# Optimization experiments

Hardware: AMD Instinct MI355X
Metric: run time of the kernel (lower is better)

## Reference

```python
import jax, jax.numpy as jnp
import numpy as np

C = 256          # input_dim
OUT = 256        # output_dim
DM = C // 4      # mamba d_model
DS = 16          # d_state
DC = 4           # d_conv
DI = 2 * DM      # d_inner (expand=2)
DTR = max(1, -(-DM // 16))  # dt_rank = ceil(d_model/16) = 4
B, Dd, H, W = 2, 8, 16, 32


def setup_inputs() -> dict:
    key = jax.random.key(0)
    ks = jax.random.split(key, 12)
    s = 0.02
    inp = {
        'x': jax.random.normal(ks[0], (B, C, Dd, H, W), jnp.float32),
        'ln_g': jnp.ones((C,), jnp.float32),
        'ln_b': jnp.zeros((C,), jnp.float32),
        'in_proj_w': jax.random.normal(ks[1], (2 * DI, DM), jnp.float32) * s,
        'conv_w': jax.random.normal(ks[2], (DI, DC), jnp.float32) * s,
        'conv_b': jnp.zeros((DI,), jnp.float32),
        'x_proj_w': jax.random.normal(ks[3], (DTR + 2 * DS, DI), jnp.float32) * s,
        'dt_proj_w': jax.random.normal(ks[4], (DI, DTR), jnp.float32) * s,
        'dt_proj_b': jax.random.uniform(ks[5], (DI,), jnp.float32, -4.0, -2.0),
        'A_log': jnp.log(jnp.broadcast_to(jnp.arange(1, DS + 1, dtype=jnp.float32), (DI, DS))),
        'D_param': jnp.ones((DI,), jnp.float32),
        'out_proj_w': jax.random.normal(ks[6], (DM, DI), jnp.float32) * s,
        'proj_w': jax.random.normal(ks[7], (OUT, C), jnp.float32) * s,
        'proj_b': jnp.zeros((OUT,), jnp.float32),
        'skip_scale': jnp.ones((1,), jnp.float32),
    }
    return inp


def _layernorm(h, g, b, eps=1e-5):
    mu = jnp.mean(h, axis=-1, keepdims=True)
    var = jnp.mean(jnp.square(h - mu), axis=-1, keepdims=True)
    return (h - mu) * jax.lax.rsqrt(var + eps) * g + b


def _mamba(xp, in_proj_w, conv_w, conv_b, x_proj_w, dt_proj_w, dt_proj_b, A_log, D_param, out_proj_w):
    # xp: (B, L, DM)
    xz = xp @ in_proj_w.T                      # (B, L, 2*DI)
    xc, z = jnp.split(xz, 2, axis=-1)
    # causal depthwise conv1d, kernel DC, left-pad DC-1
    xcT = xc.transpose(0, 2, 1)                # (B, DI, L)
    k = conv_w[:, None, :]                     # (DI, 1, DC)
    conv = jax.lax.conv_general_dilated(xcT, k, (1,), [(DC - 1, 0)], feature_group_count=DI)
    xc = jax.nn.silu(conv + conv_b[None, :, None]).transpose(0, 2, 1)  # (B, L, DI)
    x_dbl = xc @ x_proj_w.T                    # (B, L, DTR+2*DS)
    dt = x_dbl[..., :DTR]
    Bm = x_dbl[..., DTR:DTR + DS]
    Cm = x_dbl[..., DTR + DS:]
    dt = jax.nn.softplus(dt @ dt_proj_w.T + dt_proj_b)  # (B, L, DI)
    A = -jnp.exp(A_log)                        # (DI, DS)
    dA = jnp.exp(dt[..., None] * A)            # (B, L, DI, DS)
    dBx = dt[..., None] * Bm[:, :, None, :] * xc[..., None]  # (B, L, DI, DS)

    def step(h, inp):
        dA_t, dBx_t, C_t = inp
        h = dA_t * h + dBx_t                   # (B, DI, DS)
        y = jnp.einsum('bds,bs->bd', h, C_t)
        return h, y

    h0 = jnp.zeros((xp.shape[0], DI, DS), xp.dtype)
    _, ys = jax.lax.scan(step, h0, (dA.transpose(1, 0, 2, 3), dBx.transpose(1, 0, 2, 3), Cm.transpose(1, 0, 2)))
    y = ys.transpose(1, 0, 2) + D_param * xc   # (B, L, DI)
    y = y * jax.nn.silu(z)
    return y @ out_proj_w.T                    # (B, L, DM)


def reference(x, ln_g, ln_b, in_proj_w, conv_w, conv_b, x_proj_w, dt_proj_w, dt_proj_b,
              A_log, D_param, out_proj_w, proj_w, proj_b, skip_scale):
    Bb, Cc, Dd_, H_, W_ = x.shape
    L = Dd_ * H_ * W_
    xf = x.reshape(Bb, Cc, L).transpose(0, 2, 1)        # (B, L, C)
    xn = _layernorm(xf, ln_g, ln_b)
    parts = xn.reshape(Bb, L, 4, DM).transpose(2, 0, 1, 3)  # (4, B, L, DM), contiguous chunks
    mam = lambda p: _mamba(p, in_proj_w, conv_w, conv_b, x_proj_w, dt_proj_w,
                           dt_proj_b, A_log, D_param, out_proj_w)
    outs = jax.vmap(mam)(parts) + skip_scale * parts    # shared Mamba weights across chunks
    xm = outs.transpose(1, 2, 0, 3).reshape(Bb, L, Cc)
    xm = _layernorm(xm, ln_g, ln_b)                      # same LN module reused
    xp = (xm @ proj_w.T + proj_b).transpose(0, 2, 1)     # (B, OUT, L)
    return xp.reshape(Bb, -1, Dd_, H_, W_)
```

## Files before the change

### kernel.cpp

```cpp
#include <hip/hip_runtime.h>


#define B_    2
#define C_    256
#define L_    4096
#define P_    4
#define DM_   64
#define DI_   128
#define OUT_  256
#define NCH   128
#define CHL   32

__global__ __launch_bounds__(256) void k1_ln(const float* __restrict__ x,
        const float* __restrict__ g, const float* __restrict__ bb,
        float* __restrict__ xn) {
  __shared__ float tile[256][33];
  __shared__ float psum[8][32];
  __shared__ float psq[8][32];
  __shared__ float smu[32], srs[32];
  int t = threadIdx.x;
  int l0 = blockIdx.x * 32;
  int b = blockIdx.y;
  const float* xb = x + (size_t)b * C_ * L_;
  int ll = t & 31, cr = t >> 5;
  for (int i = 0; i < 32; ++i) {
    int c = cr + 8 * i;
    tile[c][ll] = xb[(size_t)c * L_ + l0 + ll];
  }
  __syncthreads();
  {
    int l = t & 31, k = t >> 5;
    float s = 0.f, sq = 0.f;
    #pragma unroll 8
    for (int j = 0; j < 32; ++j) {
      float v = tile[32 * k + j][l];
      s += v; sq += v * v;
    }
    psum[k][l] = s; psq[k][l] = sq;
  }
  __syncthreads();
  if (t < 32) {
    float s = 0.f, sq = 0.f;
    #pragma unroll
    for (int k = 0; k < 8; ++k) { s += psum[k][t]; sq += psq[k][t]; }
    float mu = s * (1.f / 256.f);
    float var = sq * (1.f / 256.f) - mu * mu;
    smu[t] = mu;
    srs[t] = rsqrtf(var + 1e-5f);
  }
  __syncthreads();
  float gc = g[t], bc = bb[t];
  for (int l = 0; l < 32; ++l) {
    float v = (tile[t][l] - smu[l]) * srs[l] * gc + bc;
    xn[((size_t)b * L_ + l0 + l) * C_ + t] = v;
  }
}

__global__ __launch_bounds__(256) void k2_inproj(const float* __restrict__ xn,
        const float* __restrict__ w, float* __restrict__ xz) {
  __shared__ float swT[32 * 256];
  __shared__ float sxT[32 * 64];
  int t = threadIdx.x;
  int l0 = blockIdx.x * 64;
  int p = blockIdx.y, b = blockIdx.z;
  int to = t & 63, tl = t >> 6;
  float acc[4][16];
  #pragma unroll
  for (int io = 0; io < 4; ++io)
    #pragma unroll
    for (int il = 0; il < 16; ++il) acc[io][il] = 0.f;

  for (int kt = 0; kt < 2; ++kt) {
    __syncthreads();
    {
      const float* wr = w + (size_t)t * 64 + kt * 32;
      #pragma unroll
      for (int k4 = 0; k4 < 8; ++k4) {
        float4 v = *(const float4*)&wr[k4 * 4];
        swT[(k4 * 4 + 0) * 256 + t] = v.x;
        swT[(k4 * 4 + 1) * 256 + t] = v.y;
        swT[(k4 * 4 + 2) * 256 + t] = v.z;
        swT[(k4 * 4 + 3) * 256 + t] = v.w;
      }
    }
    {
      int l = t & 63, dg = t >> 6;
      const float* xr = xn + ((size_t)b * L_ + l0 + l) * 256 + p * 64 + kt * 32 + dg * 8;
      #pragma unroll
      for (int jj = 0; jj < 2; ++jj) {
        float4 v = *(const float4*)&xr[jj * 4];
        sxT[(dg * 8 + jj * 4 + 0) * 64 + l] = v.x;
        sxT[(dg * 8 + jj * 4 + 1) * 64 + l] = v.y;
        sxT[(dg * 8 + jj * 4 + 2) * 64 + l] = v.z;
        sxT[(dg * 8 + jj * 4 + 3) * 64 + l] = v.w;
      }
    }
    __syncthreads();
    for (int k = 0; k < 32; ++k) {
      float4 b4 = *(const float4*)&swT[k * 256 + to * 4];
      #pragma unroll
      for (int q = 0; q < 4; ++q) {
        float4 a4 = *(const float4*)&sxT[k * 64 + tl * 16 + q * 4];
        acc[0][q*4+0] += b4.x * a4.x; acc[0][q*4+1] += b4.x * a4.y;
        acc[0][q*4+2] += b4.x * a4.z; acc[0][q*4+3] += b4.x * a4.w;
        acc[1][q*4+0] += b4.y * a4.x; acc[1][q*4+1] += b4.y * a4.y;
        acc[1][q*4+2] += b4.y * a4.z; acc[1][q*4+3] += b4.y * a4.w;
        acc[2][q*4+0] += b4.z * a4.x; acc[2][q*4+1] += b4.z * a4.y;
        acc[2][q*4+2] += b4.z * a4.z; acc[2][q*4+3] += b4.z * a4.w;
        acc[3][q*4+0] += b4.w * a4.x; acc[3][q*4+1] += b4.w * a4.y;
        acc[3][q*4+2] += b4.w * a4.z; acc[3][q*4+3] += b4.w * a4.w;
      }
    }
  }
  size_t ob = ((size_t)((b * 4 + p)) * L_ + l0 + tl * 16) * 256 + to * 4;
  #pragma unroll
  for (int il = 0; il < 16; ++il) {
    float4 v = make_float4(acc[0][il], acc[1][il], acc[2][il], acc[3][il]);
    *(float4*)&xz[ob + (size_t)il * 256] = v;
  }
}

__global__ __launch_bounds__(256) void k3_convdt(const float* __restrict__ xz,
        const float* __restrict__ conv_w, const float* __restrict__ conv_b,
        const float* __restrict__ x_proj_w, const float* __restrict__ dt_proj_w,
        const float* __restrict__ dt_proj_b,
        float* __restrict__ xc, float* __restrict__ dt, float* __restrict__ bc) {
  __shared__ float sxc[64 * 128];
  __shared__ float sdb[64 * 5];
  __shared__ float sbc[64 * 33];
  int t = threadIdx.x;
  int l0 = blockIdx.x * 64;
  int bp = blockIdx.z * P_ + blockIdx.y;
  const float* xzb = xz + (size_t)bp * L_ * 256;

  {
    int d = t & 127, lh = t >> 7;
    int lstart = l0 + lh * 32;
    float4 cw = *(const float4*)&conv_w[d * 4];
    float cb = conv_b[d];
    float w0 = (lstart >= 3) ? xzb[(size_t)(lstart - 3) * 256 + d] : 0.f;
    float w1 = (lstart >= 2) ? xzb[(size_t)(lstart - 2) * 256 + d] : 0.f;
    float w2 = (lstart >= 1) ? xzb[(size_t)(lstart - 1) * 256 + d] : 0.f;
    float* xcrow = xc + ((size_t)bp * L_ + lstart) * 128 + d;
    const float* xzrow = xzb + (size_t)lstart * 256 + d;
    #pragma unroll 4
    for (int i = 0; i < 32; ++i) {
      float w3 = xzrow[(size_t)i * 256];
      float cv = cb + cw.x * w0 + cw.y * w1 + cw.z * w2 + cw.w * w3;
      float sv = cv / (1.f + __expf(-cv));
      int row = lh * 32 + i;
      sxc[row * 128 + (d ^ (4 * (row & 31)))] = sv;
      xcrow[(size_t)i * 128] = sv;
      w0 = w1; w1 = w2; w2 = w3;
    }
  }
  __syncthreads();
  {
    int l = t & 63, og = t >> 6;
    float acc[9];
    #pragma unroll
    for (int rr = 0; rr < 9; ++rr) acc[rr] = 0.f;
    const float* wbase = x_proj_w + og * 9 * 128;
    for (int k4 = 0; k4 < 32; ++k4) {
      float4 a4 = *(const float4*)&sxc[l * 128 + ((k4 * 4) ^ (4 * (l & 31)))];
      #pragma unroll
      for (int rr = 0; rr < 9; ++rr) {
        float4 w4 = *(const float4*)&wbase[rr * 128 + k4 * 4];
        acc[rr] += a4.x * w4.x + a4.y * w4.y + a4.z * w4.z + a4.w * w4.w;
      }
    }
    #pragma unroll
    for (int rr = 0; rr < 9; ++rr) {
      int ra = og * 9 + rr;
      if (ra < 4) sdb[l * 5 + ra] = acc[rr];
      else sbc[l * 33 + (ra - 4)] = acc[rr];
    }
  }
  __syncthreads();
  #pragma unroll
  for (int i = 0; i < 8; ++i) {
    int idx = t + 256 * i;
    int row = idx >> 5, col = idx & 31;
    bc[((size_t)bp * L_ + l0 + row) * 32 + col] = sbc[row * 33 + col];
  }
  {
    int d = t & 127, lh = t >> 7;
    float4 dw = *(const float4*)&dt_proj_w[d * 4];
    float dpb = dt_proj_b[d];
    float* dtrow = dt + ((size_t)bp * L_ + l0 + lh * 32) * 128 + d;
    #pragma unroll 4
    for (int i = 0; i < 32; ++i) {
      int row = lh * 32 + i;
      float v = dpb + sdb[row * 5 + 0] * dw.x + sdb[row * 5 + 1] * dw.y
                    + sdb[row * 5 + 2] * dw.z + sdb[row * 5 + 3] * dw.w;
      float sp = (v > 20.f) ? v : log1pf(__expf(v));
      dtrow[(size_t)i * 128] = sp;
    }
  }
}

__global__ __launch_bounds__(128) void k4a_scanA(const float* __restrict__ dt,
        const float* __restrict__ xc, const float* __restrict__ bcbuf,
        const float* __restrict__ A_log,
        float* __restrict__ chA, float* __restrict__ chH) {
  int d = threadIdx.x;
  int ch = blockIdx.x, bp = blockIdx.y;
  float Av[16], h[16];
  #pragma unroll
  for (int q = 0; q < 4; ++q) {
    float4 a = *(const float4*)&A_log[d * 16 + q * 4];
    Av[q*4+0] = -__expf(a.x); Av[q*4+1] = -__expf(a.y);
    Av[q*4+2] = -__expf(a.z); Av[q*4+3] = -__expf(a.w);
  }
  #pragma unroll
  for (int s = 0; s < 16; ++s) h[s] = 0.f;
  float sumdt = 0.f;
  const float* dtp = dt + (size_t)bp * L_ * 128 + (size_t)ch * CHL * 128 + d;
  const float* xcp = xc + (size_t)bp * L_ * 128 + (size_t)ch * CHL * 128 + d;
  const float* bcp = bcbuf + (size_t)bp * L_ * 32 + (size_t)ch * CHL * 32;
  #pragma unroll 2
  for (int tt = 0; tt < CHL; ++tt) {
    float dtv = dtp[tt * 128];
    float xcv = xcp[tt * 128];
    float Bv[16];
    *(float4*)&Bv[0]  = *(const float4*)&bcp[tt * 32 + 0];
    *(float4*)&Bv[4]  = *(const float4*)&bcp[tt * 32 + 4];
    *(float4*)&Bv[8]  = *(const float4*)&bcp[tt * 32 + 8];
    *(float4*)&Bv[12] = *(const float4*)&bcp[tt * 32 + 12];
    float w = dtv * xcv;
    sumdt += dtv;
    #pragma unroll
    for (int s = 0; s < 16; ++s) {
      float dA = __expf(dtv * Av[s]);
      h[s] = fmaf(dA, h[s], w * Bv[s]);
    }
  }
  size_t o = (((size_t)bp * NCH + ch) * 128 + d) * 16;
  #pragma unroll
  for (int s = 0; s < 16; ++s) chA[o + s] = __expf(sumdt * Av[s]);
  #pragma unroll
  for (int s = 0; s < 16; ++s) chH[o + s] = h[s];
}

__global__ __launch_bounds__(256) void k4b_fold(const float* __restrict__ chA,
        float* __restrict__ chH) {
  int tid = blockIdx.x * 256 + threadIdx.x;
  int bp = tid >> 11;
  int rem = tid & 2047;
  float h = 0.f;
  for (int ch = 0; ch < NCH; ++ch) {
    size_t o = ((size_t)bp * NCH + ch) * 2048 + rem;
    float a = chA[o];
    float e = chH[o];
    chH[o] = h;
    h = fmaf(a, h, e);
  }
}

__global__ __launch_bounds__(128) void k5_scanB(const float* __restrict__ dt,
        const float* __restrict__ xc, const float* __restrict__ bcbuf,
        const float* __restrict__ xz, const float* __restrict__ A_log,
        const float* __restrict__ D_param, const float* __restrict__ chH,
        float* __restrict__ yg) {
  int d = threadIdx.x;
  int ch = blockIdx.x, bp = blockIdx.y;
  float Av[16], h[16];
  #pragma unroll
  for (int q = 0; q < 4; ++q) {
    float4 a = *(const float4*)&A_log[d * 16 + q * 4];
    Av[q*4+0] = -__expf(a.x); Av[q*4+1] = -__expf(a.y);
    Av[q*4+2] = -__expf(a.z); Av[q*4+3] = -__expf(a.w);
  }
  {
    size_t o = (((size_t)bp * NCH + ch) * 128 + d) * 16;
    #pragma unroll
    for (int q = 0; q < 4; ++q)
      *(float4*)&h[q * 4] = *(const float4*)&chH[o + q * 4];
  }
  float Dv = D_param[d];
  const float* dtp = dt + (size_t)bp * L_ * 128 + (size_t)ch * CHL * 128 + d;
  const float* xcp = xc + (size_t)bp * L_ * 128 + (size_t)ch * CHL * 128 + d;
  const float* bcp = bcbuf + (size_t)bp * L_ * 32 + (size_t)ch * CHL * 32;
  const float* zp  = xz + (size_t)bp * L_ * 256 + (size_t)ch * CHL * 256 + 128 + d;
  float* ygp = yg + (size_t)bp * L_ * 128 + (size_t)ch * CHL * 128 + d;
  #pragma unroll 2
  for (int tt = 0; tt < CHL; ++tt) {
    float dtv = dtp[tt * 128];
    float xcv = xcp[tt * 128];
    float zv  = zp[tt * 256];
    float Bv[16], Cv[16];
    *(float4*)&Bv[0]  = *(const float4*)&bcp[tt * 32 + 0];
    *(float4*)&Bv[4]  = *(const float4*)&bcp[tt * 32 + 4];
    *(float4*)&Bv[8]  = *(const float4*)&bcp[tt * 32 + 8];
    *(float4*)&Bv[12] = *(const float4*)&bcp[tt * 32 + 12];
    *(float4*)&Cv[0]  = *(const float4*)&bcp[tt * 32 + 16];
    *(float4*)&Cv[4]  = *(const float4*)&bcp[tt * 32 + 20];
    *(float4*)&Cv[8]  = *(const float4*)&bcp[tt * 32 + 24];
    *(float4*)&Cv[12] = *(const float4*)&bcp[tt * 32 + 28];
    float w = dtv * xcv;
    float r = 0.f;
    #pragma unroll
    for (int s = 0; s < 16; ++s) {
      float dA = __expf(dtv * Av[s]);
      h[s] = fmaf(dA, h[s], w * Bv[s]);
      r = fmaf(h[s], Cv[s], r);
    }
    float y = fmaf(Dv, xcv, r);
    float sig = 1.f / (1.f + __expf(-zv));
    ygp[tt * 128] = y * (zv * sig);
  }
}

__global__ __launch_bounds__(256) void k6a_gemm(const float* __restrict__ yg,
        const float* __restrict__ xn, const float* __restrict__ opw,
        const float* __restrict__ skip, float* __restrict__ xmn) {
  __shared__ float sgT[128 * 64];
  __shared__ float swT2[128 * 64];
  int t = threadIdx.x;
  int l0 = blockIdx.x * 64;
  int p = blockIdx.y, b = blockIdx.z;
  int bp = b * 4 + p;
  float sk = skip[0];
  {
    int l = t & 63, dg = t >> 6;
    const float* yr = yg + ((size_t)bp * L_ + l0 + l) * 128 + dg * 32;
    const float* wr = opw + (size_t)l * 128 + dg * 32;
    #pragma unroll
    for (int jj = 0; jj < 8; ++jj) {
      float4 v = *(const float4*)&yr[jj * 4];
      int dd = dg * 32 + jj * 4;
      sgT[(dd + 0) * 64 + l] = v.x; sgT[(dd + 1) * 64 + l] = v.y;
      sgT[(dd + 2) * 64 + l] = v.z; sgT[(dd + 3) * 64 + l] = v.w;
      float4 u = *(const float4*)&wr[jj * 4];
      swT2[(dd + 0) * 64 + l] = u.x; swT2[(dd + 1) * 64 + l] = u.y;
      swT2[(dd + 2) * 64 + l] = u.z; swT2[(dd + 3) * 64 + l] = u.w;
    }
  }
  __syncthreads();
  int to = t & 15, tl = t >> 4;
  float acc[4][4];
  #pragma unroll
  for (int io = 0; io < 4; ++io)
    #pragma unroll
    for (int il = 0; il < 4; ++il) acc[io][il] = 0.f;
  for (int dd = 0; dd < 128; ++dd) {
    float4 a4 = *(const float4*)&sgT[dd * 64 + tl * 4];
    float4 b4 = *(const float4*)&swT2[dd * 64 + to * 4];
    acc[0][0] += b4.x * a4.x; acc[0][1] += b4.x * a4.y; acc[0][2] += b4.x * a4.z; acc[0][3] += b4.x * a4.w;
    acc[1][0] += b4.y * a4.x; acc[1][1] += b4.y * a4.y; acc[1][2] += b4.y * a4.z; acc[1][3] += b4.y * a4.w;
    acc[2][0] += b4.z * a4.x; acc[2][1] += b4.z * a4.y; acc[2][2] += b4.z * a4.z; acc[2][3] += b4.z * a4.w;
    acc[3][0] += b4.w * a4.x; acc[3][1] += b4.w * a4.y; acc[3][2] += b4.w * a4.z; acc[3][3] += b4.w * a4.w;
  }
  #pragma unroll
  for (int il = 0; il < 4; ++il) {
    size_t addr = ((size_t)b * L_ + l0 + tl * 4 + il) * 256 + p * 64 + to * 4;
    float4 xv = *(const float4*)&xn[addr];
    float4 v = make_float4(acc[0][il] + sk * xv.x, acc[1][il] + sk * xv.y,
                           acc[2][il] + sk * xv.z, acc[3][il] + sk * xv.w);
    *(float4*)&xmn[addr] = v;
  }
}

__global__ __launch_bounds__(256) void k6ln(float* __restrict__ xmn,
        const float* __restrict__ g, const float* __restrict__ bb) {
  int t = threadIdx.x;
  int row = blockIdx.x * 4 + (t >> 6);
  int lane = t & 63;
  float* rp = xmn + (size_t)row * 256 + lane * 4;
  float4 v = *(const float4*)rp;
  float s = v.x + v.y + v.z + v.w;
  float q = v.x * v.x + v.y * v.y + v.z * v.z + v.w * v.w;
  #pragma unroll
  for (int off = 1; off < 64; off <<= 1) {
    s += __shfl_xor(s, off);
    q += __shfl_xor(q, off);
  }
  float mu = s * (1.f / 256.f);
  float rs = rsqrtf(q * (1.f / 256.f) - mu * mu + 1e-5f);
  float4 g4 = *(const float4*)&g[lane * 4];
  float4 b4 = *(const float4*)&bb[lane * 4];
  float4 o = make_float4((v.x - mu) * rs * g4.x + b4.x,
                         (v.y - mu) * rs * g4.y + b4.y,
                         (v.z - mu) * rs * g4.z + b4.z,
                         (v.w - mu) * rs * g4.w + b4.w);
  *(float4*)rp = o;
}

__global__ __launch_bounds__(256) void k6b_proj(const float* __restrict__ xmn,
        const float* __restrict__ pw, const float* __restrict__ pb,
        float* __restrict__ out) {
  __shared__ float saT[64 * 64];
  __shared__ float sbT[64 * 64];
  int t = threadIdx.x;
  int l0 = blockIdx.x * 64;
  int o0 = blockIdx.y * 64;
  int b = blockIdx.z;
  int to = t & 15, tl = t >> 4;
  float acc[4][4];
  #pragma unroll
  for (int io = 0; io < 4; ++io)
    #pragma unroll
    for (int il = 0; il < 4; ++il) acc[io][il] = 0.f;
  for (int kt = 0; kt < 4; ++kt) {
    __syncthreads();
    {
      int l = t & 63, cg = t >> 6;
      const float* ar = xmn + ((size_t)b * L_ + l0 + l) * 256 + kt * 64 + cg * 16;
      const float* br = pw + (size_t)(o0 + l) * 256 + kt * 64 + cg * 16;
      #pragma unroll
      for (int jj = 0; jj < 4; ++jj) {
        float4 v = *(const float4*)&ar[jj * 4];
        int cc = cg * 16 + jj * 4;
        saT[(cc + 0) * 64 + l] = v.x; saT[(cc + 1) * 64 + l] = v.y;
        saT[(cc + 2) * 64 + l] = v.z; saT[(cc + 3) * 64 + l] = v.w;
        float4 u = *(const float4*)&br[jj * 4];
        sbT[(cc + 0) * 64 + l] = u.x; sbT[(cc + 1) * 64 + l] = u.y;
        sbT[(cc + 2) * 64 + l] = u.z; sbT[(cc + 3) * 64 + l] = u.w;
      }
    }
    __syncthreads();
    for (int cc = 0; cc < 64; ++cc) {
      float4 a4 = *(const float4*)&saT[cc * 64 + tl * 4];
      float4 b4 = *(const float4*)&sbT[cc * 64 + to * 4];
      acc[0][0] += b4.x * a4.x; acc[0][1] += b4.x * a4.y; acc[0][2] += b4.x * a4.z; acc[0][3] += b4.x * a4.w;
      acc[1][0] += b4.y * a4.x; acc[1][1] += b4.y * a4.y; acc[1][2] += b4.y * a4.z; acc[1][3] += b4.y * a4.w;
      acc[2][0] += b4.z * a4.x; acc[2][1] += b4.z * a4.y; acc[2][2] += b4.z * a4.z; acc[2][3] += b4.z * a4.w;
      acc[3][0] += b4.w * a4.x; acc[3][1] += b4.w * a4.y; acc[3][2] += b4.w * a4.z; acc[3][3] += b4.w * a4.w;
    }
  }
  #pragma unroll
  for (int io = 0; io < 4; ++io) {
    int o = o0 + to * 4 + io;
    float bias = pb[o];
    float4 v = make_float4(acc[io][0] + bias, acc[io][1] + bias,
                           acc[io][2] + bias, acc[io][3] + bias);
    *(float4*)&out[((size_t)b * OUT_ + o) * L_ + l0 + tl * 4] = v;
  }
}

extern "C" void kernel_launch(void* const* d_in, const int* in_sizes, int n_in,
                              void* d_out, int out_size, void* d_ws, size_t ws_size,
                              hipStream_t stream) {
  (void)in_sizes; (void)n_in; (void)out_size; (void)ws_size;
  const float* x          = (const float*)d_in[0];
  const float* ln_g       = (const float*)d_in[1];
  const float* ln_b       = (const float*)d_in[2];
  const float* in_proj_w  = (const float*)d_in[3];
  const float* conv_w     = (const float*)d_in[4];
  const float* conv_b     = (const float*)d_in[5];
  const float* x_proj_w   = (const float*)d_in[6];
  const float* dt_proj_w  = (const float*)d_in[7];
  const float* dt_proj_b  = (const float*)d_in[8];
  const float* A_log      = (const float*)d_in[9];
  const float* D_param    = (const float*)d_in[10];
  const float* out_proj_w = (const float*)d_in[11];
  const float* proj_w     = (const float*)d_in[12];
  const float* proj_b     = (const float*)d_in[13];
  const float* skip_scale = (const float*)d_in[14];

  float* ws  = (float*)d_ws;
  float* xn  = ws;
  float* xz  = xn + 2097152;
  float* xc  = xz + 8388608;
  float* dt  = xc + 4194304;
  float* bc  = dt + 4194304;
  float* chA = bc + 1048576;
  float* chH = chA + 2097152;
  float* yg  = chH + 2097152;
  float* xmn = yg + 4194304;
  float* out = (float*)d_out;

  k1_ln<<<dim3(L_ / 32, B_), 256, 0, stream>>>(x, ln_g, ln_b, xn);
  k2_inproj<<<dim3(L_ / 64, P_, B_), 256, 0, stream>>>(xn, in_proj_w, xz);
  k3_convdt<<<dim3(L_ / 64, P_, B_), 256, 0, stream>>>(xz, conv_w, conv_b,
      x_proj_w, dt_proj_w, dt_proj_b, xc, dt, bc);
  k4a_scanA<<<dim3(NCH, B_ * P_), 128, 0, stream>>>(dt, xc, bc, A_log, chA, chH);
  k4b_fold<<<dim3(64), 256, 0, stream>>>(chA, chH);
  k5_scanB<<<dim3(NCH, B_ * P_), 128, 0, stream>>>(dt, xc, bc, xz, A_log,
      D_param, chH, yg);
  k6a_gemm<<<dim3(L_ / 64, P_, B_), 256, 0, stream>>>(yg, xn, out_proj_w,
      skip_scale, xmn);
  k6ln<<<dim3(B_ * L_ / 4), 256, 0, stream>>>(xmn, ln_g, ln_b);
  k6b_proj<<<dim3(L_ / 64, OUT_ / 64, B_), 256, 0, stream>>>(xmn, proj_w, proj_b, out);
}
```

Baseline: 234.6 us.

## Replace LDS-tiled GEMMs with row-per-thread kernels and split conv from x_proj

The in_proj, x_proj, out_proj and final projection GEMMs are rewritten so that each thread computes one row. The shared weights are read with wave-uniform addresses, which the compiler can serve as scalar or broadcast loads, and the shared-memory transposes and barriers are removed. The fused conv/x_proj/dt kernel is split into a conv kernel and a separate x_dbl kernel that also computes dt, trading an extra launch and an xc re-read for simpler kernels. LayerNorm now uses 16-position tiles with float4 loads, and fast divide and log intrinsics replace the precise ones. The risks are heavy register use from 64-wide accumulators, uncoalesced per-thread row reads in the GEMMs, and small accuracy differences from the fast math.

New measurement: 466.5 us. 98.9% more time.

```diff
diff --git a/kernel.cpp b/kernel.cpp
--- a/kernel.cpp
+++ b/kernel.cpp
@@ -14,188 +14,147 @@
 __global__ __launch_bounds__(256) void k1_ln(const float* __restrict__ x,
         const float* __restrict__ g, const float* __restrict__ bb,
         float* __restrict__ xn) {
-  __shared__ float tile[256][33];
-  __shared__ float psum[8][32];
-  __shared__ float psq[8][32];
-  __shared__ float smu[32], srs[32];
-  int t = threadIdx.x;
-  int l0 = blockIdx.x * 32;
+  __shared__ float tile[256 * 17];
+  __shared__ float reds[16 * 17];
+  __shared__ float redq[16 * 17];
+  __shared__ float smu[16], srs[16];
+  int t = threadIdx.x;
+  int l0 = blockIdx.x * 16;
   int b = blockIdx.y;
-  const float* xb = x + (size_t)b * C_ * L_;
-  int ll = t & 31, cr = t >> 5;
-  for (int i = 0; i < 32; ++i) {
-    int c = cr + 8 * i;
-    tile[c][ll] = xb[(size_t)c * L_ + l0 + ll];
+  const float* xb = x + ((size_t)b * C_ + t) * L_ + l0;
+  #pragma unroll
+  for (int i = 0; i < 4; ++i) {
+    float4 u = *(const float4*)&xb[i * 4];
+    tile[t * 17 + i * 4 + 0] = u.x;
+    tile[t * 17 + i * 4 + 1] = u.y;
+    tile[t * 17 + i * 4 + 2] = u.z;
+    tile[t * 17 + i * 4 + 3] = u.w;
   }
   __syncthreads();
   {
-    int l = t & 31, k = t >> 5;
-    float s = 0.f, sq = 0.f;
-    #pragma unroll 8
-    for (int j = 0; j < 32; ++j) {
-      float v = tile[32 * k + j][l];
-      s += v; sq += v * v;
-    }
-    psum[k][l] = s; psq[k][l] = sq;
+    int l = t & 15, kg = t >> 4;
+    float s = 0.f, q = 0.f;
+    #pragma unroll
+    for (int j = 0; j < 16; ++j) {
+      float v = tile[(kg * 16 + j) * 17 + l];
+      s += v; q += v * v;
+    }
+    reds[kg * 17 + l] = s;
+    redq[kg * 17 + l] = q;
   }
   __syncthreads();
-  if (t < 32) {
-    float s = 0.f, sq = 0.f;
-    #pragma unroll
-    for (int k = 0; k < 8; ++k) { s += psum[k][t]; sq += psq[k][t]; }
+  if (t < 16) {
+    float s = 0.f, q = 0.f;
+    #pragma unroll
+    for (int kg = 0; kg < 16; ++kg) { s += reds[kg * 17 + t]; q += redq[kg * 17 + t]; }
     float mu = s * (1.f / 256.f);
-    float var = sq * (1.f / 256.f) - mu * mu;
     smu[t] = mu;
-    srs[t] = rsqrtf(var + 1e-5f);
+    srs[t] = rsqrtf(q * (1.f / 256.f) - mu * mu + 1e-5f);
   }
   __syncthreads();
   float gc = g[t], bc = bb[t];
-  for (int l = 0; l < 32; ++l) {
-    float v = (tile[t][l] - smu[l]) * srs[l] * gc + bc;
+  #pragma unroll
+  for (int l = 0; l < 16; ++l) {
+    float v = (tile[t * 17 + l] - smu[l]) * srs[l] * gc + bc;
     xn[((size_t)b * L_ + l0 + l) * C_ + t] = v;
   }
 }
 
-__global__ __launch_bounds__(256) void k2_inproj(const float* __restrict__ xn,
+__global__ __launch_bounds__(64) void k2_inproj(const float* __restrict__ xn,
         const float* __restrict__ w, float* __restrict__ xz) {
-  __shared__ float swT[32 * 256];
-  __shared__ float sxT[32 * 64];
-  int t = threadIdx.x;
-  int l0 = blockIdx.x * 64;
-  int p = blockIdx.y, b = blockIdx.z;
-  int to = t & 63, tl = t >> 6;
-  float acc[4][16];
-  #pragma unroll
-  for (int io = 0; io < 4; ++io)
-    #pragma unroll
-    for (int il = 0; il < 16; ++il) acc[io][il] = 0.f;
-
-  for (int kt = 0; kt < 2; ++kt) {
-    __syncthreads();
-    {
-      const float* wr = w + (size_t)t * 64 + kt * 32;
-      #pragma unroll
-      for (int k4 = 0; k4 < 8; ++k4) {
-        float4 v = *(const float4*)&wr[k4 * 4];
-        swT[(k4 * 4 + 0) * 256 + t] = v.x;
-        swT[(k4 * 4 + 1) * 256 + t] = v.y;
-        swT[(k4 * 4 + 2) * 256 + t] = v.z;
-        swT[(k4 * 4 + 3) * 256 + t] = v.w;
-      }
-    }
-    {
-      int l = t & 63, dg = t >> 6;
-      const float* xr = xn + ((size_t)b * L_ + l0 + l) * 256 + p * 64 + kt * 32 + dg * 8;
-      #pragma unroll
-      for (int jj = 0; jj < 2; ++jj) {
-        float4 v = *(const float4*)&xr[jj * 4];
-        sxT[(dg * 8 + jj * 4 + 0) * 64 + l] = v.x;
-        sxT[(dg * 8 + jj * 4 + 1) * 64 + l] = v.y;
-        sxT[(dg * 8 + jj * 4 + 2) * 64 + l] = v.z;
-        sxT[(dg * 8 + jj * 4 + 3) * 64 + l] = v.w;
-      }
-    }
-    __syncthreads();
-    for (int k = 0; k < 32; ++k) {
-      float4 b4 = *(const float4*)&swT[k * 256 + to * 4];
-      #pragma unroll
-      for (int q = 0; q < 4; ++q) {
-        float4 a4 = *(const float4*)&sxT[k * 64 + tl * 16 + q * 4];
-        acc[0][q*4+0] += b4.x * a4.x; acc[0][q*4+1] += b4.x * a4.y;
-        acc[0][q*4+2] += b4.x * a4.z; acc[0][q*4+3] += b4.x * a4.w;
-        acc[1][q*4+0] += b4.y * a4.x; acc[1][q*4+1] += b4.y * a4.y;
-        acc[1][q*4+2] += b4.y * a4.z; acc[1][q*4+3] += b4.y * a4.w;
-        acc[2][q*4+0] += b4.z * a4.x; acc[2][q*4+1] += b4.z * a4.y;
-        acc[2][q*4+2] += b4.z * a4.z; acc[2][q*4+3] += b4.z * a4.w;
-        acc[3][q*4+0] += b4.w * a4.x; acc[3][q*4+1] += b4.w * a4.y;
-        acc[3][q*4+2] += b4.w * a4.z; acc[3][q*4+3] += b4.w * a4.w;
-      }
-    }
-  }
-  size_t ob = ((size_t)((b * 4 + p)) * L_ + l0 + tl * 16) * 256 + to * 4;
-  #pragma unroll
-  for (int il = 0; il < 16; ++il) {
-    float4 v = make_float4(acc[0][il], acc[1][il], acc[2][il], acc[3][il]);
-    *(float4*)&xz[ob + (size_t)il * 256] = v;
-  }
-}
-
-__global__ __launch_bounds__(256) void k3_convdt(const float* __restrict__ xz,
+  int t = threadIdx.x;
+  int row = blockIdx.x * 64 + t;
+  int o0 = blockIdx.y * 64;
+  int bp = row >> 12, l = row & 4095, b = bp >> 2, p = bp & 3;
+  const float* xr = xn + ((size_t)b * L_ + l) * 256 + p * 64;
+  float acc[64];
+  #pragma unroll
+  for (int oo = 0; oo < 64; ++oo) acc[oo] = 0.f;
+  #pragma unroll 2
+  for (int k4 = 0; k4 < 16; ++k4) {
+    float4 a4 = *(const float4*)&xr[k4 * 4];
+    const float* wp = w + (size_t)o0 * 64 + k4 * 4;
+    #pragma unroll
+    for (int oo = 0; oo < 64; ++oo) {
+      float4 w4 = *(const float4*)&wp[(size_t)oo * 64];
+      acc[oo] += a4.x * w4.x + a4.y * w4.y + a4.z * w4.z + a4.w * w4.w;
+    }
+  }
+  float* orow = xz + (size_t)row * 256 + o0;
+  #pragma unroll
+  for (int q = 0; q < 16; ++q) {
+    float4 v = make_float4(acc[q * 4 + 0], acc[q * 4 + 1], acc[q * 4 + 2], acc[q * 4 + 3]);
+    *(float4*)&orow[q * 4] = v;
+  }
+}
+
+__global__ __launch_bounds__(256) void k3a_conv(const float* __restrict__ xz,
         const float* __restrict__ conv_w, const float* __restrict__ conv_b,
+        float* __restrict__ xc) {
+  int t = threadIdx.x;
+  int d = t & 127, lh = t >> 7;
+  int bp = blockIdx.y;
+  int lstart = blockIdx.x * 32 + lh * 16;
+  const float* xzb = xz + (size_t)bp * L_ * 256;
+  float4 cw = *(const float4*)&conv_w[d * 4];
+  float cb = conv_b[d];
+  float w0 = (lstart >= 3) ? xzb[(size_t)(lstart - 3) * 256 + d] : 0.f;
+  float w1 = (lstart >= 2) ? xzb[(size_t)(lstart - 2) * 256 + d] : 0.f;
+  float w2 = (lstart >= 1) ? xzb[(size_t)(lstart - 1) * 256 + d] : 0.f;
+  const float* xzrow = xzb + (size_t)lstart * 256 + d;
+  float* xcrow = xc + ((size_t)bp * L_ + lstart) * 128 + d;
+  #pragma unroll 4
+  for (int i = 0; i < 16; ++i) {
+    float w3 = xzrow[(size_t)i * 256];
+    float cv = cb + cw.x * w0 + cw.y * w1 + cw.z * w2 + cw.w * w3;
+    float sv = __fdividef(cv, 1.f + __expf(-cv));
+    xcrow[(size_t)i * 128] = sv;
+    w0 = w1; w1 = w2; w2 = w3;
+  }
+}
+
+__global__ __launch_bounds__(64) void k3b_xdbl(const float* __restrict__ xc,
         const float* __restrict__ x_proj_w, const float* __restrict__ dt_proj_w,
         const float* __restrict__ dt_proj_b,
-        float* __restrict__ xc, float* __restrict__ dt, float* __restrict__ bc) {
-  __shared__ float sxc[64 * 128];
-  __shared__ float sdb[64 * 5];
-  __shared__ float sbc[64 * 33];
-  int t = threadIdx.x;
-  int l0 = blockIdx.x * 64;
-  int bp = blockIdx.z * P_ + blockIdx.y;
-  const float* xzb = xz + (size_t)bp * L_ * 256;
-
-  {
-    int d = t & 127, lh = t >> 7;
-    int lstart = l0 + lh * 32;
-    float4 cw = *(const float4*)&conv_w[d * 4];
-    float cb = conv_b[d];
-    float w0 = (lstart >= 3) ? xzb[(size_t)(lstart - 3) * 256 + d] : 0.f;
-    float w1 = (lstart >= 2) ? xzb[(size_t)(lstart - 2) * 256 + d] : 0.f;
-    float w2 = (lstart >= 1) ? xzb[(size_t)(lstart - 1) * 256 + d] : 0.f;
-    float* xcrow = xc + ((size_t)bp * L_ + lstart) * 128 + d;
-    const float* xzrow = xzb + (size_t)lstart * 256 + d;
-    #pragma unroll 4
-    for (int i = 0; i < 32; ++i) {
-      float w3 = xzrow[(size_t)i * 256];
-      float cv = cb + cw.x * w0 + cw.y * w1 + cw.z * w2 + cw.w * w3;
-      float sv = cv / (1.f + __expf(-cv));
-      int row = lh * 32 + i;
-      sxc[row * 128 + (d ^ (4 * (row & 31)))] = sv;
-      xcrow[(size_t)i * 128] = sv;
-      w0 = w1; w1 = w2; w2 = w3;
-    }
-  }
-  __syncthreads();
-  {
-    int l = t & 63, og = t >> 6;
-    float acc[9];
-    #pragma unroll
-    for (int rr = 0; rr < 9; ++rr) acc[rr] = 0.f;
-    const float* wbase = x_proj_w + og * 9 * 128;
-    for (int k4 = 0; k4 < 32; ++k4) {
-      float4 a4 = *(const float4*)&sxc[l * 128 + ((k4 * 4) ^ (4 * (l & 31)))];
+        float* __restrict__ bc, float* __restrict__ dt) {
+  int t = threadIdx.x;
+  int row = blockIdx.x * 64 + t;
+  int rh = blockIdx.y;
+  const float* ar = xc + (size_t)row * 128;
+  float acc[18];
+  #pragma unroll
+  for (int rr = 0; rr < 18; ++rr) acc[rr] = 0.f;
+  #pragma unroll 2
+  for (int k4 = 0; k4 < 32; ++k4) {
+    float4 a4 = *(const float4*)&ar[k4 * 4];
+    const float* wp = x_proj_w + rh * 18 * 128 + k4 * 4;
+    #pragma unroll
+    for (int rr = 0; rr < 18; ++rr) {
+      float4 w4 = *(const float4*)&wp[rr * 128];
+      acc[rr] += a4.x * w4.x + a4.y * w4.y + a4.z * w4.z + a4.w * w4.w;
+    }
+  }
+  if (rh == 0) {
+    #pragma unroll
+    for (int rr = 4; rr < 18; ++rr) bc[(size_t)row * 32 + (rr - 4)] = acc[rr];
+    float* dtr = dt + (size_t)row * 128;
+    #pragma unroll 2
+    for (int d4 = 0; d4 < 32; ++d4) {
+      float4 o;
       #pragma unroll
-      for (int rr = 0; rr < 9; ++rr) {
-        float4 w4 = *(const float4*)&wbase[rr * 128 + k4 * 4];
-        acc[rr] += a4.x * w4.x + a4.y * w4.y + a4.z * w4.z + a4.w * w4.w;
+      for (int j = 0; j < 4; ++j) {
+        int dd = d4 * 4 + j;
+        float4 w4 = *(const float4*)&dt_proj_w[dd * 4];
+        float v = dt_proj_b[dd] + acc[0] * w4.x + acc[1] * w4.y
+                                + acc[2] * w4.z + acc[3] * w4.w;
+        float sp = (v > 20.f) ? v : __logf(1.f + __expf(v));
+        (&o.x)[j] = sp;
       }
-    }
-    #pragma unroll
-    for (int rr = 0; rr < 9; ++rr) {
-      int ra = og * 9 + rr;
-      if (ra < 4) sdb[l * 5 + ra] = acc[rr];
-      else sbc[l * 33 + (ra - 4)] = acc[rr];
-    }
-  }
-  __syncthreads();
-  #pragma unroll
-  for (int i = 0; i < 8; ++i) {
-    int idx = t + 256 * i;
-    int row = idx >> 5, col = idx & 31;
-    bc[((size_t)bp * L_ + l0 + row) * 32 + col] = sbc[row * 33 + col];
-  }
-  {
-    int d = t & 127, lh = t >> 7;
-    float4 dw = *(const float4*)&dt_proj_w[d * 4];
-    float dpb = dt_proj_b[d];
-    float* dtrow = dt + ((size_t)bp * L_ + l0 + lh * 32) * 128 + d;
-    #pragma unroll 4
-    for (int i = 0; i < 32; ++i) {
-      int row = lh * 32 + i;
-      float v = dpb + sdb[row * 5 + 0] * dw.x + sdb[row * 5 + 1] * dw.y
-                    + sdb[row * 5 + 2] * dw.z + sdb[row * 5 + 3] * dw.w;
-      float sp = (v > 20.f) ? v : log1pf(__expf(v));
-      dtrow[(size_t)i * 128] = sp;
-    }
+      *(float4*)&dtr[d4 * 4] = o;
+    }
+  } else {
+    #pragma unroll
+    for (int rr = 0; rr < 18; ++rr) bc[(size_t)row * 32 + 14 + rr] = acc[rr];
   }
 }
 
@@ -306,58 +265,40 @@
       r = fmaf(h[s], Cv[s], r);
     }
     float y = fmaf(Dv, xcv, r);
-    float sig = 1.f / (1.f + __expf(-zv));
+    float sig = __fdividef(1.f, 1.f + __expf(-zv));
     ygp[tt * 128] = y * (zv * sig);
   }
 }
 
-__global__ __launch_bounds__(256) void k6a_gemm(const float* __restrict__ yg,
+__global__ __launch_bounds__(64) void k6a_gemm(const float* __restrict__ yg,
         const float* __restrict__ xn, const float* __restrict__ opw,
         const float* __restrict__ skip, float* __restrict__ xmn) {
-  __shared__ float sgT[128 * 64];
-  __shared__ float swT2[128 * 64];
-  int t = threadIdx.x;
-  int l0 = blockIdx.x * 64;
-  int p = blockIdx.y, b = blockIdx.z;
-  int bp = b * 4 + p;
+  int t = threadIdx.x;
+  int row = blockIdx.x * 64 + t;
+  int oh = blockIdx.y;
+  int bp = row >> 12, l = row & 4095, b = bp >> 2, p = bp & 3;
+  const float* ar = yg + (size_t)row * 128;
+  float acc[32];
+  #pragma unroll
+  for (int rr = 0; rr < 32; ++rr) acc[rr] = 0.f;
+  #pragma unroll 2
+  for (int k4 = 0; k4 < 32; ++k4) {
+    float4 a4 = *(const float4*)&ar[k4 * 4];
+    const float* wp = opw + (size_t)(oh * 32) * 128 + k4 * 4;
+    #pragma unroll
+    for (int rr = 0; rr < 32; ++rr) {
+      float4 w4 = *(const float4*)&wp[rr * 128];
+      acc[rr] += a4.x * w4.x + a4.y * w4.y + a4.z * w4.z + a4.w * w4.w;
+    }
+  }
   float sk = skip[0];
-  {
-    int l = t & 63, dg = t >> 6;
-    const float* yr = yg + ((size_t)bp * L_ + l0 + l) * 128 + dg * 32;
-    const float* wr = opw + (size_t)l * 128 + dg * 32;
-    #pragma unroll
-    for (int jj = 0; jj < 8; ++jj) {
-      float4 v = *(const float4*)&yr[jj * 4];
-      int dd = dg * 32 + jj * 4;
-      sgT[(dd + 0) * 64 + l] = v.x; sgT[(dd + 1) * 64 + l] = v.y;
-      sgT[(dd + 2) * 64 + l] = v.z; sgT[(dd + 3) * 64 + l] = v.w;
-      float4 u = *(const float4*)&wr[jj * 4];
-      swT2[(dd + 0) * 64 + l] = u.x; swT2[(dd + 1) * 64 + l] = u.y;
-      swT2[(dd + 2) * 64 + l] = u.z; swT2[(dd + 3) * 64 + l] = u.w;
-    }
-  }
-  __syncthreads();
-  int to = t & 15, tl = t >> 4;
-  float acc[4][4];
-  #pragma unroll
-  for (int io = 0; io < 4; ++io)
-    #pragma unroll
-    for (int il = 0; il < 4; ++il) acc[io][il] = 0.f;
-  for (int dd = 0; dd < 128; ++dd) {
-    float4 a4 = *(const float4*)&sgT[dd * 64 + tl * 4];
-    float4 b4 = *(const float4*)&swT2[dd * 64 + to * 4];
-    acc[0][0] += b4.x * a4.x; acc[0][1] += b4.x * a4.y; acc[0][2] += b4.x * a4.z; acc[0][3] += b4.x * a4.w;
-    acc[1][0] += b4.y * a4.x; acc[1][1] += b4.y * a4.y; acc[1][2] += b4.y * a4.z; acc[1][3] += b4.y * a4.w;
-    acc[2][0] += b4.z * a4.x; acc[2][1] += b4.z * a4.y; acc[2][2] += b4.z * a4.z; acc[2][3] += b4.z * a4.w;
-    acc[3][0] += b4.w * a4.x; acc[3][1] += b4.w * a4.y; acc[3][2] += b4.w * a4.z; acc[3][3] += b4.w * a4.w;
-  }
-  #pragma unroll
-  for (int il = 0; il < 4; ++il) {
-    size_t addr = ((size_t)b * L_ + l0 + tl * 4 + il) * 256 + p * 64 + to * 4;
-    float4 xv = *(const float4*)&xn[addr];
-    float4 v = make_float4(acc[0][il] + sk * xv.x, acc[1][il] + sk * xv.y,
-                           acc[2][il] + sk * xv.z, acc[3][il] + sk * xv.w);
-    *(float4*)&xmn[addr] = v;
+  size_t base = ((size_t)b * L_ + l) * 256 + p * 64 + oh * 32;
+  #pragma unroll
+  for (int q = 0; q < 8; ++q) {
+    float4 xv = *(const float4*)&xn[base + q * 4];
+    float4 v = make_float4(acc[q*4+0] + sk * xv.x, acc[q*4+1] + sk * xv.y,
+                           acc[q*4+2] + sk * xv.z, acc[q*4+3] + sk * xv.w);
+    *(float4*)&xmn[base + q * 4] = v;
   }
 }
 
@@ -386,55 +327,30 @@
   *(float4*)rp = o;
 }
 
-__global__ __launch_bounds__(256) void k6b_proj(const float* __restrict__ xmn,
+__global__ __launch_bounds__(64) void k6b_proj(const float* __restrict__ xmn,
         const float* __restrict__ pw, const float* __restrict__ pb,
         float* __restrict__ out) {
-  __shared__ float saT[64 * 64];
-  __shared__ float sbT[64 * 64];
-  int t = threadIdx.x;
-  int l0 = blockIdx.x * 64;
-  int o0 = blockIdx.y * 64;
-  int b = blockIdx.z;
-  int to = t & 15, tl = t >> 4;
-  float acc[4][4];
-  #pragma unroll
-  for (int io = 0; io < 4; ++io)
-    #pragma unroll
-    for (int il = 0; il < 4; ++il) acc[io][il] = 0.f;
-  for (int kt = 0; kt < 4; ++kt) {
-    __syncthreads();
-    {
-      int l = t & 63, cg = t >> 6;
-      const float* ar = xmn + ((size_t)b * L_ + l0 + l) * 256 + kt * 64 + cg * 16;
-      const float* br = pw + (size_t)(o0 + l) * 256 + kt * 64 + cg * 16;
-      #pragma unroll
-      for (int jj = 0; jj < 4; ++jj) {
-        float4 v = *(const float4*)&ar[jj * 4];
-        int cc = cg * 16 + jj * 4;
-        saT[(cc + 0) * 64 + l] = v.x; saT[(cc + 1) * 64 + l] = v.y;
-        saT[(cc + 2) * 64 + l] = v.z; saT[(cc + 3) * 64 + l] = v.w;
-        float4 u = *(const float4*)&br[jj * 4];
-        sbT[(cc + 0) * 64 + l] = u.x; sbT[(cc + 1) * 64 + l] = u.y;
-        sbT[(cc + 2) * 64 + l] = u.z; sbT[(cc + 3) * 64 + l] = u.w;
-      }
-    }
-    __syncthreads();
-    for (int cc = 0; cc < 64; ++cc) {
-      float4 a4 = *(const float4*)&saT[cc * 64 + tl * 4];
-      float4 b4 = *(const float4*)&sbT[cc * 64 + to * 4];
-      acc[0][0] += b4.x * a4.x; acc[0][1] += b4.x * a4.y; acc[0][2] += b4.x * a4.z; acc[0][3] += b4.x * a4.w;
-      acc[1][0] += b4.y * a4.x; acc[1][1] += b4.y * a4.y; acc[1][2] += b4.y * a4.z; acc[1][3] += b4.y * a4.w;
-      acc[2][0] += b4.z * a4.x; acc[2][1] += b4.z * a4.y; acc[2][2] += b4.z * a4.z; acc[2][3] += b4.z * a4.w;
-      acc[3][0] += b4.w * a4.x; acc[3][1] += b4.w * a4.y; acc[3][2] += b4.w * a4.z; acc[3][3] += b4.w * a4.w;
-    }
-  }
-  #pragma unroll
-  for (int io = 0; io < 4; ++io) {
-    int o = o0 + to * 4 + io;
-    float bias = pb[o];
-    float4 v = make_float4(acc[io][0] + bias, acc[io][1] + bias,
-                           acc[io][2] + bias, acc[io][3] + bias);
-    *(float4*)&out[((size_t)b * OUT_ + o) * L_ + l0 + tl * 4] = v;
+  int t = threadIdx.x;
+  int row = blockIdx.x * 64 + t;
+  int o0 = blockIdx.y * 32;
+  int b = row >> 12, l = row & 4095;
+  const float* ar = xmn + (size_t)row * 256;
+  float acc[32];
+  #pragma unroll
+  for (int oo = 0; oo < 32; ++oo) acc[oo] = 0.f;
+  #pragma unroll 2
+  for (int k4 = 0; k4 < 64; ++k4) {
+    float4 a4 = *(const float4*)&ar[k4 * 4];
+    const float* wp = pw + (size_t)o0 * 256 + k4 * 4;
+    #pragma unroll
+    for (int oo = 0; oo < 32; ++oo) {
+      float4 w4 = *(const float4*)&wp[(size_t)oo * 256];
+      acc[oo] += a4.x * w4.x + a4.y * w4.y + a4.z * w4.z + a4.w * w4.w;
+    }
+  }
+  #pragma unroll
+  for (int oo = 0; oo < 32; ++oo) {
+    out[((size_t)b * OUT_ + o0 + oo) * L_ + l] = acc[oo] + pb[o0 + oo];
   }
 }
 
@@ -470,16 +386,17 @@
   float* xmn = yg + 4194304;
   float* out = (float*)d_out;
 
-  k1_ln<<<dim3(L_ / 32, B_), 256, 0, stream>>>(x, ln_g, ln_b, xn);
-  k2_inproj<<<dim3(L_ / 64, P_, B_), 256, 0, stream>>>(xn, in_proj_w, xz);
-  k3_convdt<<<dim3(L_ / 64, P_, B_), 256, 0, stream>>>(xz, conv_w, conv_b,
-      x_proj_w, dt_proj_w, dt_proj_b, xc, dt, bc);
+  k1_ln<<<dim3(L_ / 16, B_), 256, 0, stream>>>(x, ln_g, ln_b, xn);
+  k2_inproj<<<dim3(512, 4), 64, 0, stream>>>(xn, in_proj_w, xz);
+  k3a_conv<<<dim3(128, B_ * P_), 256, 0, stream>>>(xz, conv_w, conv_b, xc);
+  k3b_xdbl<<<dim3(512, 2), 64, 0, stream>>>(xc, x_proj_w, dt_proj_w,
+      dt_proj_b, bc, dt);
   k4a_scanA<<<dim3(NCH, B_ * P_), 128, 0, stream>>>(dt, xc, bc, A_log, chA, chH);
   k4b_fold<<<dim3(64), 256, 0, stream>>>(chA, chH);
   k5_scanB<<<dim3(NCH, B_ * P_), 128, 0, stream>>>(dt, xc, bc, xz, A_log,
       D_param, chH, yg);
-  k6a_gemm<<<dim3(L_ / 64, P_, B_), 256, 0, stream>>>(yg, xn, out_proj_w,
+  k6a_gemm<<<dim3(512, 2), 64, 0, stream>>>(yg, xn, out_proj_w,
       skip_scale, xmn);
   k6ln<<<dim3(B_ * L_ / 4), 256, 0, stream>>>(xmn, ln_g, ln_b);
-  k6b_proj<<<dim3(L_ / 64, OUT_ / 64, B_), 256, 0, stream>>>(xmn, proj_w, proj_b, out);
-}
+  k6b_proj<<<dim3(128, 8), 64, 0, stream>>>(xmn, proj_w, proj_b, out);
+}
```
